# Kernel optimization log

Measured on AMD Instinct MI355X. Metric: run time of the kernel, lower is better.

The kernel has to match this reference:

```python
import jax, jax.numpy as jnp
import numpy as np

W_REG = 3.0
N_CAND = 4
IOU_LEN = 15.0
BIG_COST = 1e8


def focal_cost(cls_pred, gt_labels, alpha=0.25, gamma=2.0, eps=1e-12):
    # cls_pred: [B,P,C] logits, gt_labels: [B,T] int -> [B,P,T]
    p = jax.nn.sigmoid(cls_pred)
    neg = -jnp.log(1.0 - p + eps) * (1.0 - alpha) * p ** gamma
    pos = -jnp.log(p + eps) * alpha * (1.0 - p) ** gamma
    B, P, _ = cls_pred.shape
    T = gt_labels.shape[1]
    idx = jnp.broadcast_to(gt_labels[:, None, :], (B, P, T))
    return jnp.take_along_axis(pos, idx, axis=2) - jnp.take_along_axis(neg, idx, axis=2)


def line_iou(pred, target, img_w, length=IOU_LEN):
    # pred: [B,P,O], target: [B,T,O] -> [B,P,T] (unaligned)
    px1, px2 = pred - length, pred + length
    tx1, tx2 = target - length, target + length
    ovr = jnp.minimum(px2[:, :, None, :], tx2[:, None, :, :]) - jnp.maximum(px1[:, :, None, :], tx1[:, None, :, :])
    union = jnp.maximum(px2[:, :, None, :], tx2[:, None, :, :]) - jnp.minimum(px1[:, :, None, :], tx1[:, None, :, :])
    invalid = ((target < 0) | (target >= img_w))[:, None, :, :]
    ovr = jnp.where(invalid, 0.0, ovr)
    union = jnp.where(invalid, 0.0, union)
    return ovr.sum(-1) / (union.sum(-1) + 1e-9)


def clrnet_assign(preds, targets, masks, img_w, img_h):
    B, P, _ = preds.shape
    T = targets.shape[1]
    w = float(img_w - 1)
    h = float(img_h - 1)
    pa = preds.at[..., 3].multiply(w).at[..., 6:].multiply(w)
    ta = targets.at[..., 3].multiply(w).at[..., 6:].multiply(w)
    p_off, t_off = pa[..., 6:], ta[..., 6:]

    # --- distance score (masked mean L1 over valid target x-offsets) ---
    tvalid = (t_off >= 0) & (t_off < img_w)                      # [B,T,O]
    cmask = tvalid[:, None, :, :]                                 # [B,1,T,O]
    clen = jnp.maximum(cmask.sum(-1).astype(pa.dtype), 1.0)      # [B,1,T]
    diff = jnp.abs(p_off[:, :, None, :] - t_off[:, None, :, :]) * cmask  # [B,P,T,O]
    distances = diff.sum(-1) / clen                               # [B,P,T]
    dist_max = jnp.maximum(distances.max(axis=(1, 2), keepdims=True), 1e-8)
    dist_score = 1.0 - distances / dist_max + 0.01

    # --- start-point score (euclidean on (y*(h), x)) ---
    ps = pa[..., 2:4].at[..., 0].multiply(h)
    ts = ta[..., 2:4].at[..., 0].multiply(h)
    start_d = jnp.sqrt(((ps[:, :, None, :] - ts[:, None, :, :]) ** 2).sum(-1))
    start_max = jnp.maximum(start_d.max(axis=(1, 2), keepdims=True), 1e-8)
    start_score = 1.0 - start_d / start_max + 0.01

    # --- theta score ---
    th_d = jnp.abs(pa[..., 4][:, :, None] - ta[..., 4][:, None, :]) * 180.0
    th_max = jnp.maximum(th_d.max(axis=(1, 2), keepdims=True), 1e-8)
    th_score = 1.0 - th_d / th_max + 0.01

    # --- total cost ---
    gt_labels = ta[..., 1].astype(jnp.int32)
    cls_cost = focal_cost(pa[..., :2], gt_labels)
    reg = (jnp.maximum(dist_score, 1e-3) * jnp.maximum(start_score, 1e-3)
           * jnp.maximum(th_score, 1e-3))
    total_cost = -(reg ** 2) * W_REG + cls_cost                   # [B,P,T]
    valid_t = (masks > 0)[:, None, :]                             # [B,1,T]
    total_cost = jnp.where(valid_t, total_cost, BIG_COST)

    # --- dynamic-k from line IoU ---
    liou = jnp.nan_to_num(line_iou(p_off, t_off, img_w), nan=0.0)
    liou = jnp.where(valid_t, liou, 0.0)
    k = min(N_CAND, P)
    topk_ious, _ = jax.lax.top_k(jnp.swapaxes(liou, 1, 2), k)     # [B,T,k]
    dynamic_ks = jnp.maximum(topk_ious.sum(-1).astype(jnp.int32), 1)
    dynamic_ks = jnp.where(masks > 0, dynamic_ks, 0)              # [B,T]

    # --- top-k lowest-cost priors per target, scatter into matching matrix ---
    _, topk_idx = jax.lax.top_k(-jnp.swapaxes(total_cost, 1, 2), k)  # [B,T,k]
    sel = (jnp.arange(k)[None, None, :] < dynamic_ks[:, :, None]).astype(total_cost.dtype)  # [B,T,k]
    one_hot_p = jax.nn.one_hot(topk_idx, P, dtype=total_cost.dtype)  # [B,T,k,P]
    matching = jnp.swapaxes((one_hot_p * sel[..., None]).sum(2), 1, 2)  # [B,P,T]

    # --- conflict resolution: a prior matched to >1 targets keeps argmin-cost one ---
    conflict = matching.sum(-1) > 1                               # [B,P]
    masked_cost = jnp.where(matching == 0, jnp.inf, total_cost)
    best_t = jnp.argmin(masked_cost, axis=2)                      # [B,P]
    new_m = jax.nn.one_hot(best_t, T, dtype=matching.dtype)
    matching = jnp.where(conflict[..., None], new_m, matching)

    has_match = matching.sum(-1) > 0.5
    t_idx = jnp.argmax(matching, axis=2)
    matched = jnp.where(has_match, t_idx, -1).astype(jnp.int32)
    return matched >= 0, matched


def setup_inputs() -> dict:
    key = jax.random.key(0)
    k1, k2, k3 = jax.random.split(key, 3)
    B, P, T, O = 32, 1000, 16, 72
    D = 6 + O
    preds = jax.random.uniform(k1, (B, P, D), dtype=jnp.float32)
    # slightly outside [0,1] so the invalid-offset masking path is exercised
    targets = jax.random.uniform(k2, (B, T, D), dtype=jnp.float32, minval=-0.05, maxval=1.05)
    masks = jax.random.randint(k3, (B, T), 0, 2).astype(jnp.int32)
    return {"preds": preds, "targets": targets, "masks": masks, "img_w": 800, "img_h": 320}


def reference(preds, targets, masks, img_w, img_h):
    return clrnet_assign(preds, targets, masks, img_w, img_h)
```

## Files before the change

kernel.cpp:

```cpp
#include <hip/hip_runtime.h>
#include <math.h>

#define B_ 32
#define P_ 1000
#define T_ 16
#define D_ 78
#define O_ 72
#define NXB 16
#define BIGC 100000000.0f

__global__ __launch_bounds__(256) void k1(
        const float* __restrict__ preds, const float* __restrict__ targets,
        const int* __restrict__ imgw_p, const int* __restrict__ imgh_p,
        float* __restrict__ Sarr, float4* __restrict__ scal4, float* __restrict__ pths,
        float* __restrict__ pmax, float* __restrict__ cntg) {
    __shared__ float pred_s[64 * 81];
    __shared__ float2 tomg[T_ * O_];
    __shared__ float wmax[4][3];
    __shared__ float cnt_s[T_], clen_s[T_], ts0_s[T_], ts1_s[T_], tth_s[T_];

    const int b = blockIdx.y, bx = blockIdx.x;
    const int p0 = bx * 64;
    const int rows = min(64, P_ - p0);
    const int tid = threadIdx.x;
    const float w = (float)(imgw_p[0] - 1);
    const float h = (float)(imgh_p[0] - 1);
    const float imgwf = (float)imgw_p[0];

    {
        const float4* gbase = (const float4*)(preds + ((size_t)b * P_ + p0) * D_);
        const int n4 = rows * D_ / 4;
        for (int i = tid; i < n4; i += 256) {
            float4 v = gbase[i];
            int base = i * 4;
            int r = base / D_, c = base - r * D_;
#pragma unroll
            for (int k = 0; k < 4; ++k) {
                int cc = c + k, rr = r;
                if (cc >= D_) { cc -= D_; ++rr; }
                float x = (&v.x)[k];
                if (cc >= 6 || cc == 3) x *= w;
                pred_s[rr * 81 + cc] = x;
            }
        }
    }
    for (int i = tid; i < T_ * O_; i += 256) {
        int t = i / O_, o = i - t * O_;
        float to = targets[((size_t)b * T_ + t) * D_ + 6 + o] * w;
        float m = (to >= 0.f && to < imgwf) ? 1.f : 0.f;
        tomg[((t >> 2) * O_ + o) * 4 + (t & 3)] = make_float2(to, m);
    }
    __syncthreads();
    if (tid < T_) {
        int t = tid;
        float c = 0.f;
        for (int o = 0; o < O_; ++o) c += tomg[((t >> 2) * O_ + o) * 4 + (t & 3)].y;
        cnt_s[t] = c;
        clen_s[t] = fmaxf(c, 1.f);
        const float* tr = targets + ((size_t)b * T_ + t) * D_;
        ts0_s[t] = tr[2] * h;
        ts1_s[t] = tr[3] * w;
        tth_s[t] = tr[4];
    }
    __syncthreads();

    if (bx == 0 && tid < T_) cntg[b * T_ + tid] = cnt_s[tid];

    const int lane = tid & 63;
    const int tg = tid >> 6;
    const int p = p0 + lane;

    float ldm = 0.f, lsm = 0.f, ltm = 0.f;
    if (p < P_) {
        const float* lrow = pred_s + lane * 81;
        const float4* tg4 = (const float4*)(tomg + (size_t)tg * O_ * 4);
        float S0 = 0.f, S1 = 0.f, S2 = 0.f, S3 = 0.f;
#pragma unroll 4
        for (int o = 0; o < O_; ++o) {
            float po = lrow[6 + o];
            float4 r0 = tg4[2 * o];
            float4 r1 = tg4[2 * o + 1];
            S0 += r0.y * fabsf(po - r0.x);
            S1 += r0.w * fabsf(po - r0.z);
            S2 += r1.y * fabsf(po - r1.x);
            S3 += r1.w * fabsf(po - r1.z);
        }
        float Sv[4] = {S0, S1, S2, S3};
        float ps0 = lrow[2] * h, ps1 = lrow[3], pth = lrow[4];
#pragma unroll
        for (int j = 0; j < 4; ++j) {
            int t = 4 * tg + j;
            float S = Sv[j];
            Sarr[(size_t)(b * T_ + t) * P_ + p] = S;
            float dv = S / clen_s[t];
            ldm = fmaxf(ldm, dv);
            float d0 = ps0 - ts0_s[t], d1 = ps1 - ts1_s[t];
            lsm = fmaxf(lsm, sqrtf(d0 * d0 + d1 * d1));
            ltm = fmaxf(ltm, fabsf(pth - tth_s[t]) * 180.f);
        }
        if (tg == 0) {
            float fc[2];
#pragma unroll
            for (int c = 0; c < 2; ++c) {
                float x = lrow[c];
                float pc = 1.f / (1.f + expf(-x));
                float neg = -logf(1.f - pc + 1e-12f) * 0.75f * pc * pc;
                float pos = -logf(pc + 1e-12f) * 0.25f * (1.f - pc) * (1.f - pc);
                fc[c] = pos - neg;
            }
            scal4[(size_t)b * P_ + p] = make_float4(fc[0], fc[1], ps0, ps1);
            pths[(size_t)b * P_ + p] = pth;
        }
    }

    for (int off = 32; off; off >>= 1) {
        ldm = fmaxf(ldm, __shfl_xor(ldm, off, 64));
        lsm = fmaxf(lsm, __shfl_xor(lsm, off, 64));
        ltm = fmaxf(ltm, __shfl_xor(ltm, off, 64));
    }
    if (lane == 0) { wmax[tg][0] = ldm; wmax[tg][1] = lsm; wmax[tg][2] = ltm; }
    __syncthreads();
    if (tid == 0) {
        float m0 = 0.f, m1 = 0.f, m2 = 0.f;
#pragma unroll
        for (int i = 0; i < 4; ++i) {
            m0 = fmaxf(m0, wmax[i][0]);
            m1 = fmaxf(m1, wmax[i][1]);
            m2 = fmaxf(m2, wmax[i][2]);
        }
        float* q = pmax + (size_t)(b * NXB + bx) * 3;
        q[0] = m0; q[1] = m1; q[2] = m2;
    }
}

__global__ __launch_bounds__(256) void k2(
        const float* __restrict__ targets, const int* __restrict__ masks,
        const int* __restrict__ imgw_p, const int* __restrict__ imgh_p,
        const float* __restrict__ Sarr,
        const float4* __restrict__ scal4, const float* __restrict__ pths,
        const float* __restrict__ pmax, const float* __restrict__ cntg,
        int4* __restrict__ sel, float4* __restrict__ selc) {
    __shared__ float costL[1024];
    __shared__ float SL[1024];

    const int wid = blockIdx.x;
    const int b = wid >> 4, t = wid & 15;
    const int tid = threadIdx.x;

    float dm = 0.f, sm = 0.f, tm = 0.f;
    for (int i = 0; i < NXB; ++i) {
        const float* q = pmax + (size_t)(b * NXB + i) * 3;
        dm = fmaxf(dm, q[0]); sm = fmaxf(sm, q[1]); tm = fmaxf(tm, q[2]);
    }
    dm = fmaxf(dm, 1e-8f); sm = fmaxf(sm, 1e-8f); tm = fmaxf(tm, 1e-8f);

    const float w = (float)(imgw_p[0] - 1);
    const float h = (float)(imgh_p[0] - 1);
    const float* tr = targets + (size_t)(b * T_ + t) * D_;
    const float ts0 = tr[2] * h, ts1 = tr[3] * w, tth = tr[4];
    int lab = (int)tr[1]; lab = lab < 0 ? 0 : (lab > 1 ? 1 : lab);
    const int mk = masks[b * T_ + t];
    const float cntv = cntg[b * T_ + t];
    const float clen = fmaxf(cntv, 1.f);
    const float c30 = 30.f * cntv;

    const float* Srow = Sarr + (size_t)(b * T_ + t) * P_;
    const float4* s4b = scal4 + (size_t)b * P_;
    const float* ptb = pths + (size_t)b * P_;

#pragma unroll
    for (int i = 0; i < 4; ++i) {
        int p = tid + 256 * i;
        if (p < P_) {
            float S = Srow[p];
            float4 s4 = s4b[p];
            float pth = ptb[p];
            float dv = S / clen;
            float dsc = 1.f - dv / dm + 0.01f;
            float d0 = s4.z - ts0, d1 = s4.w - ts1;
            float ssc = 1.f - sqrtf(d0 * d0 + d1 * d1) / sm + 0.01f;
            float tsc = 1.f - fabsf(pth - tth) * 180.f / tm + 0.01f;
            float reg = fmaxf(dsc, 1e-3f) * fmaxf(ssc, 1e-3f) * fmaxf(tsc, 1e-3f);
            float c = -(reg * reg) * 3.f + (lab ? s4.y : s4.x);
            if (mk <= 0) c = BIGC;
            costL[p] = c;
            SL[p] = S;
        } else {
            costL[p] = INFINITY;
            SL[p] = INFINITY;
        }
    }
    __syncthreads();
    if (tid >= 64) return;

    const int lane = tid;

    float v0, v1, v2, v3;
#define SROUND(vr) { float bv = INFINITY; int bi = 0x7fffffff;            \
        _Pragma("unroll")                                                 \
        for (int i = 0; i < 16; ++i) { int ix = lane + 64 * i;            \
            float v = SL[ix];                                             \
            if (v < bv || (v == bv && ix < bi)) { bv = v; bi = ix; } }    \
        for (int off = 32; off; off >>= 1) {                              \
            float ov = __shfl_xor(bv, off, 64);                           \
            int oi = __shfl_xor(bi, off, 64);                             \
            if (ov < bv || (ov == bv && oi < bi)) { bv = ov; bi = oi; }   \
        }                                                                 \
        vr = bv; if ((bi & 63) == lane) SL[bi] = INFINITY; }
    SROUND(v0) SROUND(v1) SROUND(v2) SROUND(v3)
#undef SROUND
    float l0 = (c30 - v0) / (c30 + v0 + 1e-9f);
    float l1 = (c30 - v1) / (c30 + v1 + 1e-9f);
    float l2 = (c30 - v2) / (c30 + v2 + 1e-9f);
    float l3 = (c30 - v3) / (c30 + v3 + 1e-9f);
    float sum = ((l0 + l1) + l2) + l3;
    int dk = 0;
    if (mk > 0) {
        dk = (int)sum;
        if (dk < 1) dk = 1;
        if (dk > 4) dk = 4;
    }

    int s0, s1, s2, s3;
    float c0, c1, c2, c3;
#define CROUND(sr, cr) { float bv = INFINITY; int bi = 0x7fffffff;        \
        _Pragma("unroll")                                                 \
        for (int i = 0; i < 16; ++i) { int ix = lane + 64 * i;            \
            float v = costL[ix];                                          \
            if (v < bv || (v == bv && ix < bi)) { bv = v; bi = ix; } }    \
        for (int off = 32; off; off >>= 1) {                              \
            float ov = __shfl_xor(bv, off, 64);                           \
            int oi = __shfl_xor(bi, off, 64);                             \
            if (ov < bv || (ov == bv && oi < bi)) { bv = ov; bi = oi; }   \
        }                                                                 \
        sr = bi; cr = bv; if ((bi & 63) == lane) costL[bi] = INFINITY; }
    CROUND(s0, c0) CROUND(s1, c1) CROUND(s2, c2) CROUND(s3, c3)
#undef CROUND

    if (lane == 0) {
        sel[wid]  = make_int4(dk > 0 ? s0 : -1, dk > 1 ? s1 : -1,
                              dk > 2 ? s2 : -1, dk > 3 ? s3 : -1);
        selc[wid] = make_float4(c0, c1, c2, c3);
    }
}

__global__ __launch_bounds__(256) void k3(const int* __restrict__ sel,
                                          const float* __restrict__ selc,
                                          int* __restrict__ out) {
    __shared__ int selE[64];
    __shared__ float selC[64];
    const int b = blockIdx.y, cx = blockIdx.x;
    if (threadIdx.x < 64) {
        selE[threadIdx.x] = sel[b * 64 + threadIdx.x];
        selC[threadIdx.x] = selc[b * 64 + threadIdx.x];
    }
    __syncthreads();

    const int p = cx * 250 + threadIdx.x;
    if (threadIdx.x < 250) {
        int matched = -1;
        float best = INFINITY;
#pragma unroll
        for (int t = 0; t < T_; ++t) {
#pragma unroll
            for (int j = 0; j < 4; ++j) {
                if (selE[4 * t + j] == p) {
                    float c = selC[4 * t + j];
                    if (c < best) { best = c; matched = t; }
                }
            }
        }
        out[b * P_ + p] = (matched >= 0) ? 1 : 0;
        out[B_ * P_ + b * P_ + p] = matched;
    }
}

extern "C" void kernel_launch(void* const* d_in, const int* in_sizes, int n_in,
                              void* d_out, int out_size, void* d_ws, size_t ws_size,
                              hipStream_t stream) {
    const float* preds   = (const float*)d_in[0];
    const float* targets = (const float*)d_in[1];
    const int*   masks   = (const int*)d_in[2];
    const int*   imgw    = (const int*)d_in[3];
    const int*   imgh    = (const int*)d_in[4];
    int* out = (int*)d_out;

    char* ws = (char*)d_ws;
    float*  Sarr  = (float*)ws;
    float4* scal4 = (float4*)(ws + 2048000);
    float*  pths  = (float*)(ws + 2560000);
    float*  pmax  = (float*)(ws + 2688000);
    float*  cntg  = (float*)(ws + 2694144);
    int4*   sel   = (int4*)(ws + 2696192);
    float4* selc  = (float4*)(ws + 2704384);

    k1<<<dim3(NXB, B_), 256, 0, stream>>>(preds, targets, imgw, imgh,
                                          Sarr, scal4, pths, pmax, cntg);
    k2<<<B_ * T_, 256, 0, stream>>>(targets, masks, imgw, imgh, Sarr, scal4, pths,
                                    pmax, cntg, sel, selc);
    k3<<<dim3(4, B_), 256, 0, stream>>>((const int*)sel, (const float*)selc, out);
}
```

Measured before the change: 35.38 us.

## Fuse three kernels into one cooperative kernel with grid-wide syncs

```diff
diff --git a/kernel.cpp b/kernel.cpp
--- a/kernel.cpp
+++ b/kernel.cpp
@@ -1,5 +1,8 @@
 #include <hip/hip_runtime.h>
+#include <hip/hip_cooperative_groups.h>
 #include <math.h>
+
+namespace cg = cooperative_groups;
 
 #define B_ 32
 #define P_ 1000
@@ -9,269 +12,275 @@
 #define NXB 16
 #define BIGC 100000000.0f
 
-__global__ __launch_bounds__(256) void k1(
+__global__ __launch_bounds__(256, 2) void kfused(
         const float* __restrict__ preds, const float* __restrict__ targets,
+        const int* __restrict__ masks,
         const int* __restrict__ imgw_p, const int* __restrict__ imgh_p,
         float* __restrict__ Sarr, float4* __restrict__ scal4, float* __restrict__ pths,
-        float* __restrict__ pmax, float* __restrict__ cntg) {
-    __shared__ float pred_s[64 * 81];
-    __shared__ float2 tomg[T_ * O_];
-    __shared__ float wmax[4][3];
-    __shared__ float cnt_s[T_], clen_s[T_], ts0_s[T_], ts1_s[T_], tth_s[T_];
-
-    const int b = blockIdx.y, bx = blockIdx.x;
-    const int p0 = bx * 64;
-    const int rows = min(64, P_ - p0);
+        float* __restrict__ pmax, float* __restrict__ cntg,
+        int4* __restrict__ sel, float4* __restrict__ selc,
+        int* __restrict__ out) {
+    cg::grid_group grid = cg::this_grid();
+    __shared__ __align__(16) float smem[8192];
+
+    const int g = blockIdx.x;
     const int tid = threadIdx.x;
     const float w = (float)(imgw_p[0] - 1);
     const float h = (float)(imgh_p[0] - 1);
-    const float imgwf = (float)imgw_p[0];
 
     {
-        const float4* gbase = (const float4*)(preds + ((size_t)b * P_ + p0) * D_);
-        const int n4 = rows * D_ / 4;
-        for (int i = tid; i < n4; i += 256) {
-            float4 v = gbase[i];
-            int base = i * 4;
-            int r = base / D_, c = base - r * D_;
-#pragma unroll
-            for (int k = 0; k < 4; ++k) {
-                int cc = c + k, rr = r;
-                if (cc >= D_) { cc -= D_; ++rr; }
-                float x = (&v.x)[k];
-                if (cc >= 6 || cc == 3) x *= w;
-                pred_s[rr * 81 + cc] = x;
-            }
+        float*  pred_s = smem;
+        float2* tomg   = (float2*)(smem + 5184);
+        float*  cnt_s  = smem + 5184 + 2304;
+        float*  clen_s = cnt_s + 16;
+        float*  ts0_s  = clen_s + 16;
+        float*  ts1_s  = ts0_s + 16;
+        float*  tth_s  = ts1_s + 16;
+        float*  wmaxf  = tth_s + 16;
+
+        const int b = g >> 4, bx = g & 15;
+        const int p0 = bx * 64;
+        const int rows = min(64, P_ - p0);
+        const float imgwf = (float)imgw_p[0];
+
+        {
+            const float4* gbase = (const float4*)(preds + ((size_t)b * P_ + p0) * D_);
+            const int n4 = rows * D_ / 4;
+            for (int i = tid; i < n4; i += 256) {
+                float4 v = gbase[i];
+                int base = i * 4;
+                int r = base / D_, c = base - r * D_;
+#pragma unroll
+                for (int k = 0; k < 4; ++k) {
+                    int cc = c + k, rr = r;
+                    if (cc >= D_) { cc -= D_; ++rr; }
+                    float x = (&v.x)[k];
+                    if (cc >= 6 || cc == 3) x *= w;
+                    pred_s[rr * 81 + cc] = x;
+                }
+            }
+        }
+        for (int i = tid; i < T_ * O_; i += 256) {
+            int t = i / O_, o = i - t * O_;
+            float to = targets[((size_t)b * T_ + t) * D_ + 6 + o] * w;
+            float m = (to >= 0.f && to < imgwf) ? 1.f : 0.f;
+            tomg[((t >> 2) * O_ + o) * 4 + (t & 3)] = make_float2(to, m);
+        }
+        __syncthreads();
+        if (tid < T_) {
+            int t = tid;
+            float c = 0.f;
+            for (int o = 0; o < O_; ++o) c += tomg[((t >> 2) * O_ + o) * 4 + (t & 3)].y;
+            cnt_s[t] = c;
+            clen_s[t] = fmaxf(c, 1.f);
+            const float* tr = targets + ((size_t)b * T_ + t) * D_;
+            ts0_s[t] = tr[2] * h;
+            ts1_s[t] = tr[3] * w;
+            tth_s[t] = tr[4];
+        }
+        __syncthreads();
+
+        if (bx == 0 && tid < T_) cntg[b * T_ + tid] = cnt_s[tid];
+
+        const int lane = tid & 63;
+        const int tg = tid >> 6;
+        const int p = p0 + lane;
+
+        float ldm = 0.f, lsm = 0.f, ltm = 0.f;
+        if (p < P_) {
+            const float* lrow = pred_s + lane * 81;
+            const float4* tg4 = (const float4*)(tomg + (size_t)tg * O_ * 4);
+            float S0 = 0.f, S1 = 0.f, S2 = 0.f, S3 = 0.f;
+#pragma unroll 4
+            for (int o = 0; o < O_; ++o) {
+                float po = lrow[6 + o];
+                float4 r0 = tg4[2 * o];
+                float4 r1 = tg4[2 * o + 1];
+                S0 += r0.y * fabsf(po - r0.x);
+                S1 += r0.w * fabsf(po - r0.z);
+                S2 += r1.y * fabsf(po - r1.x);
+                S3 += r1.w * fabsf(po - r1.z);
+            }
+            float Sv[4] = {S0, S1, S2, S3};
+            float ps0 = lrow[2] * h, ps1 = lrow[3], pth = lrow[4];
+#pragma unroll
+            for (int j = 0; j < 4; ++j) {
+                int t = 4 * tg + j;
+                float S = Sv[j];
+                Sarr[(size_t)(b * T_ + t) * P_ + p] = S;
+                float dv = S / clen_s[t];
+                ldm = fmaxf(ldm, dv);
+                float d0 = ps0 - ts0_s[t], d1 = ps1 - ts1_s[t];
+                lsm = fmaxf(lsm, sqrtf(d0 * d0 + d1 * d1));
+                ltm = fmaxf(ltm, fabsf(pth - tth_s[t]) * 180.f);
+            }
+            if (tg == 0) {
+                float fc[2];
+#pragma unroll
+                for (int c = 0; c < 2; ++c) {
+                    float x = lrow[c];
+                    float pc = 1.f / (1.f + expf(-x));
+                    float neg = -logf(1.f - pc + 1e-12f) * 0.75f * pc * pc;
+                    float pos = -logf(pc + 1e-12f) * 0.25f * (1.f - pc) * (1.f - pc);
+                    fc[c] = pos - neg;
+                }
+                scal4[(size_t)b * P_ + p] = make_float4(fc[0], fc[1], ps0, ps1);
+                pths[(size_t)b * P_ + p] = pth;
+            }
+        }
+
+        for (int off = 32; off; off >>= 1) {
+            ldm = fmaxf(ldm, __shfl_xor(ldm, off, 64));
+            lsm = fmaxf(lsm, __shfl_xor(lsm, off, 64));
+            ltm = fmaxf(ltm, __shfl_xor(ltm, off, 64));
+        }
+        if (lane == 0) { wmaxf[tg * 3 + 0] = ldm; wmaxf[tg * 3 + 1] = lsm; wmaxf[tg * 3 + 2] = ltm; }
+        __syncthreads();
+        if (tid == 0) {
+            float m0 = 0.f, m1 = 0.f, m2 = 0.f;
+#pragma unroll
+            for (int i = 0; i < 4; ++i) {
+                m0 = fmaxf(m0, wmaxf[i * 3 + 0]);
+                m1 = fmaxf(m1, wmaxf[i * 3 + 1]);
+                m2 = fmaxf(m2, wmaxf[i * 3 + 2]);
+            }
+            float* q = pmax + (size_t)(b * NXB + bx) * 3;
+            q[0] = m0; q[1] = m1; q[2] = m2;
         }
     }
-    for (int i = tid; i < T_ * O_; i += 256) {
-        int t = i / O_, o = i - t * O_;
-        float to = targets[((size_t)b * T_ + t) * D_ + 6 + o] * w;
-        float m = (to >= 0.f && to < imgwf) ? 1.f : 0.f;
-        tomg[((t >> 2) * O_ + o) * 4 + (t & 3)] = make_float2(to, m);
+
+    grid.sync();
+
+    {
+        float* costL = smem;
+        float* SL    = smem + 1024;
+
+        const int b = g >> 4, t = g & 15;
+
+        float dm = 0.f, sm = 0.f, tm = 0.f;
+        for (int i = 0; i < NXB; ++i) {
+            const float* q = pmax + (size_t)(b * NXB + i) * 3;
+            dm = fmaxf(dm, q[0]); sm = fmaxf(sm, q[1]); tm = fmaxf(tm, q[2]);
+        }
+        dm = fmaxf(dm, 1e-8f); sm = fmaxf(sm, 1e-8f); tm = fmaxf(tm, 1e-8f);
+
+        const float* tr = targets + (size_t)(b * T_ + t) * D_;
+        const float ts0 = tr[2] * h, ts1 = tr[3] * w, tth = tr[4];
+        int lab = (int)tr[1]; lab = lab < 0 ? 0 : (lab > 1 ? 1 : lab);
+        const int mk = masks[b * T_ + t];
+        const float cntv = cntg[b * T_ + t];
+        const float clen = fmaxf(cntv, 1.f);
+        const float c30 = 30.f * cntv;
+
+        const float* Srow = Sarr + (size_t)(b * T_ + t) * P_;
+        const float4* s4b = scal4 + (size_t)b * P_;
+        const float* ptb = pths + (size_t)b * P_;
+
+#pragma unroll
+        for (int i = 0; i < 4; ++i) {
+            int p = tid + 256 * i;
+            if (p < P_) {
+                float S = Srow[p];
+                float4 s4 = s4b[p];
+                float pth = ptb[p];
+                float dv = S / clen;
+                float dsc = 1.f - dv / dm + 0.01f;
+                float d0 = s4.z - ts0, d1 = s4.w - ts1;
+                float ssc = 1.f - sqrtf(d0 * d0 + d1 * d1) / sm + 0.01f;
+                float tsc = 1.f - fabsf(pth - tth) * 180.f / tm + 0.01f;
+                float reg = fmaxf(dsc, 1e-3f) * fmaxf(ssc, 1e-3f) * fmaxf(tsc, 1e-3f);
+                float c = -(reg * reg) * 3.f + (lab ? s4.y : s4.x);
+                if (mk <= 0) c = BIGC;
+                costL[p] = c;
+                SL[p] = S;
+            } else {
+                costL[p] = INFINITY;
+                SL[p] = INFINITY;
+            }
+        }
+        __syncthreads();
+
+        if (tid < 64) {
+            const int lane = tid;
+
+            float v0, v1, v2, v3;
+#define SROUND(vr) { float bv = INFINITY; int bi = 0x7fffffff;            \
+            _Pragma("unroll")                                             \
+            for (int i = 0; i < 16; ++i) { int ix = lane + 64 * i;        \
+                float v = SL[ix];                                         \
+                if (v < bv || (v == bv && ix < bi)) { bv = v; bi = ix; } }\
+            for (int off = 32; off; off >>= 1) {                          \
+                float ov = __shfl_xor(bv, off, 64);                       \
+                int oi = __shfl_xor(bi, off, 64);                         \
+                if (ov < bv || (ov == bv && oi < bi)) { bv = ov; bi = oi; } } \
+            vr = bv; if ((bi & 63) == lane) SL[bi] = INFINITY; }
+            SROUND(v0) SROUND(v1) SROUND(v2) SROUND(v3)
+#undef SROUND
+            float l0 = (c30 - v0) / (c30 + v0 + 1e-9f);
+            float l1 = (c30 - v1) / (c30 + v1 + 1e-9f);
+            float l2 = (c30 - v2) / (c30 + v2 + 1e-9f);
+            float l3 = (c30 - v3) / (c30 + v3 + 1e-9f);
+            float sum = ((l0 + l1) + l2) + l3;
+            int dk = 0;
+            if (mk > 0) {
+                dk = (int)sum;
+                if (dk < 1) dk = 1;
+                if (dk > 4) dk = 4;
+            }
+
+            int s0, s1, s2, s3;
+            float c0, c1, c2, c3;
+#define CROUND(sr, cr) { float bv = INFINITY; int bi = 0x7fffffff;        \
+            _Pragma("unroll")                                             \
+            for (int i = 0; i < 16; ++i) { int ix = lane + 64 * i;        \
+                float v = costL[ix];                                      \
+                if (v < bv || (v == bv && ix < bi)) { bv = v; bi = ix; } }\
+            for (int off = 32; off; off >>= 1) {                          \
+                float ov = __shfl_xor(bv, off, 64);                       \
+                int oi = __shfl_xor(bi, off, 64);                         \
+                if (ov < bv || (ov == bv && oi < bi)) { bv = ov; bi = oi; } } \
+            sr = bi; cr = bv; if ((bi & 63) == lane) costL[bi] = INFINITY; }
+            CROUND(s0, c0) CROUND(s1, c1) CROUND(s2, c2) CROUND(s3, c3)
+#undef CROUND
+
+            if (lane == 0) {
+                sel[g]  = make_int4(dk > 0 ? s0 : -1, dk > 1 ? s1 : -1,
+                                    dk > 2 ? s2 : -1, dk > 3 ? s3 : -1);
+                selc[g] = make_float4(c0, c1, c2, c3);
+            }
+        }
     }
-    __syncthreads();
-    if (tid < T_) {
-        int t = tid;
-        float c = 0.f;
-        for (int o = 0; o < O_; ++o) c += tomg[((t >> 2) * O_ + o) * 4 + (t & 3)].y;
-        cnt_s[t] = c;
-        clen_s[t] = fmaxf(c, 1.f);
-        const float* tr = targets + ((size_t)b * T_ + t) * D_;
-        ts0_s[t] = tr[2] * h;
-        ts1_s[t] = tr[3] * w;
-        tth_s[t] = tr[4];
-    }
-    __syncthreads();
-
-    if (bx == 0 && tid < T_) cntg[b * T_ + tid] = cnt_s[tid];
-
-    const int lane = tid & 63;
-    const int tg = tid >> 6;
-    const int p = p0 + lane;
-
-    float ldm = 0.f, lsm = 0.f, ltm = 0.f;
-    if (p < P_) {
-        const float* lrow = pred_s + lane * 81;
-        const float4* tg4 = (const float4*)(tomg + (size_t)tg * O_ * 4);
-        float S0 = 0.f, S1 = 0.f, S2 = 0.f, S3 = 0.f;
-#pragma unroll 4
-        for (int o = 0; o < O_; ++o) {
-            float po = lrow[6 + o];
-            float4 r0 = tg4[2 * o];
-            float4 r1 = tg4[2 * o + 1];
-            S0 += r0.y * fabsf(po - r0.x);
-            S1 += r0.w * fabsf(po - r0.z);
-            S2 += r1.y * fabsf(po - r1.x);
-            S3 += r1.w * fabsf(po - r1.z);
-        }
-        float Sv[4] = {S0, S1, S2, S3};
-        float ps0 = lrow[2] * h, ps1 = lrow[3], pth = lrow[4];
-#pragma unroll
-        for (int j = 0; j < 4; ++j) {
-            int t = 4 * tg + j;
-            float S = Sv[j];
-            Sarr[(size_t)(b * T_ + t) * P_ + p] = S;
-            float dv = S / clen_s[t];
-            ldm = fmaxf(ldm, dv);
-            float d0 = ps0 - ts0_s[t], d1 = ps1 - ts1_s[t];
-            lsm = fmaxf(lsm, sqrtf(d0 * d0 + d1 * d1));
-            ltm = fmaxf(ltm, fabsf(pth - tth_s[t]) * 180.f);
-        }
-        if (tg == 0) {
-            float fc[2];
-#pragma unroll
-            for (int c = 0; c < 2; ++c) {
-                float x = lrow[c];
-                float pc = 1.f / (1.f + expf(-x));
-                float neg = -logf(1.f - pc + 1e-12f) * 0.75f * pc * pc;
-                float pos = -logf(pc + 1e-12f) * 0.25f * (1.f - pc) * (1.f - pc);
-                fc[c] = pos - neg;
-            }
-            scal4[(size_t)b * P_ + p] = make_float4(fc[0], fc[1], ps0, ps1);
-            pths[(size_t)b * P_ + p] = pth;
-        }
-    }
-
-    for (int off = 32; off; off >>= 1) {
-        ldm = fmaxf(ldm, __shfl_xor(ldm, off, 64));
-        lsm = fmaxf(lsm, __shfl_xor(lsm, off, 64));
-        ltm = fmaxf(ltm, __shfl_xor(ltm, off, 64));
-    }
-    if (lane == 0) { wmax[tg][0] = ldm; wmax[tg][1] = lsm; wmax[tg][2] = ltm; }
-    __syncthreads();
-    if (tid == 0) {
-        float m0 = 0.f, m1 = 0.f, m2 = 0.f;
-#pragma unroll
-        for (int i = 0; i < 4; ++i) {
-            m0 = fmaxf(m0, wmax[i][0]);
-            m1 = fmaxf(m1, wmax[i][1]);
-            m2 = fmaxf(m2, wmax[i][2]);
-        }
-        float* q = pmax + (size_t)(b * NXB + bx) * 3;
-        q[0] = m0; q[1] = m1; q[2] = m2;
-    }
-}
-
-__global__ __launch_bounds__(256) void k2(
-        const float* __restrict__ targets, const int* __restrict__ masks,
-        const int* __restrict__ imgw_p, const int* __restrict__ imgh_p,
-        const float* __restrict__ Sarr,
-        const float4* __restrict__ scal4, const float* __restrict__ pths,
-        const float* __restrict__ pmax, const float* __restrict__ cntg,
-        int4* __restrict__ sel, float4* __restrict__ selc) {
-    __shared__ float costL[1024];
-    __shared__ float SL[1024];
-
-    const int wid = blockIdx.x;
-    const int b = wid >> 4, t = wid & 15;
-    const int tid = threadIdx.x;
-
-    float dm = 0.f, sm = 0.f, tm = 0.f;
-    for (int i = 0; i < NXB; ++i) {
-        const float* q = pmax + (size_t)(b * NXB + i) * 3;
-        dm = fmaxf(dm, q[0]); sm = fmaxf(sm, q[1]); tm = fmaxf(tm, q[2]);
-    }
-    dm = fmaxf(dm, 1e-8f); sm = fmaxf(sm, 1e-8f); tm = fmaxf(tm, 1e-8f);
-
-    const float w = (float)(imgw_p[0] - 1);
-    const float h = (float)(imgh_p[0] - 1);
-    const float* tr = targets + (size_t)(b * T_ + t) * D_;
-    const float ts0 = tr[2] * h, ts1 = tr[3] * w, tth = tr[4];
-    int lab = (int)tr[1]; lab = lab < 0 ? 0 : (lab > 1 ? 1 : lab);
-    const int mk = masks[b * T_ + t];
-    const float cntv = cntg[b * T_ + t];
-    const float clen = fmaxf(cntv, 1.f);
-    const float c30 = 30.f * cntv;
-
-    const float* Srow = Sarr + (size_t)(b * T_ + t) * P_;
-    const float4* s4b = scal4 + (size_t)b * P_;
-    const float* ptb = pths + (size_t)b * P_;
-
-#pragma unroll
-    for (int i = 0; i < 4; ++i) {
-        int p = tid + 256 * i;
-        if (p < P_) {
-            float S = Srow[p];
-            float4 s4 = s4b[p];
-            float pth = ptb[p];
-            float dv = S / clen;
-            float dsc = 1.f - dv / dm + 0.01f;
-            float d0 = s4.z - ts0, d1 = s4.w - ts1;
-            float ssc = 1.f - sqrtf(d0 * d0 + d1 * d1) / sm + 0.01f;
-            float tsc = 1.f - fabsf(pth - tth) * 180.f / tm + 0.01f;
-            float reg = fmaxf(dsc, 1e-3f) * fmaxf(ssc, 1e-3f) * fmaxf(tsc, 1e-3f);
-            float c = -(reg * reg) * 3.f + (lab ? s4.y : s4.x);
-            if (mk <= 0) c = BIGC;
-            costL[p] = c;
-            SL[p] = S;
-        } else {
-            costL[p] = INFINITY;
-            SL[p] = INFINITY;
-        }
-    }
-    __syncthreads();
-    if (tid >= 64) return;
-
-    const int lane = tid;
-
-    float v0, v1, v2, v3;
-#define SROUND(vr) { float bv = INFINITY; int bi = 0x7fffffff;            \
-        _Pragma("unroll")                                                 \
-        for (int i = 0; i < 16; ++i) { int ix = lane + 64 * i;            \
-            float v = SL[ix];                                             \
-            if (v < bv || (v == bv && ix < bi)) { bv = v; bi = ix; } }    \
-        for (int off = 32; off; off >>= 1) {                              \
-            float ov = __shfl_xor(bv, off, 64);                           \
-            int oi = __shfl_xor(bi, off, 64);                             \
-            if (ov < bv || (ov == bv && oi < bi)) { bv = ov; bi = oi; }   \
-        }                                                                 \
-        vr = bv; if ((bi & 63) == lane) SL[bi] = INFINITY; }
-    SROUND(v0) SROUND(v1) SROUND(v2) SROUND(v3)
-#undef SROUND
-    float l0 = (c30 - v0) / (c30 + v0 + 1e-9f);
-    float l1 = (c30 - v1) / (c30 + v1 + 1e-9f);
-    float l2 = (c30 - v2) / (c30 + v2 + 1e-9f);
-    float l3 = (c30 - v3) / (c30 + v3 + 1e-9f);
-    float sum = ((l0 + l1) + l2) + l3;
-    int dk = 0;
-    if (mk > 0) {
-        dk = (int)sum;
-        if (dk < 1) dk = 1;
-        if (dk > 4) dk = 4;
-    }
-
-    int s0, s1, s2, s3;
-    float c0, c1, c2, c3;
-#define CROUND(sr, cr) { float bv = INFINITY; int bi = 0x7fffffff;        \
-        _Pragma("unroll")                                                 \
-        for (int i = 0; i < 16; ++i) { int ix = lane + 64 * i;            \
-            float v = costL[ix];                                          \
-            if (v < bv || (v == bv && ix < bi)) { bv = v; bi = ix; } }    \
-        for (int off = 32; off; off >>= 1) {                              \
-            float ov = __shfl_xor(bv, off, 64);                           \
-            int oi = __shfl_xor(bi, off, 64);                             \
-            if (ov < bv || (ov == bv && oi < bi)) { bv = ov; bi = oi; }   \
-        }                                                                 \
-        sr = bi; cr = bv; if ((bi & 63) == lane) costL[bi] = INFINITY; }
-    CROUND(s0, c0) CROUND(s1, c1) CROUND(s2, c2) CROUND(s3, c3)
-#undef CROUND
-
-    if (lane == 0) {
-        sel[wid]  = make_int4(dk > 0 ? s0 : -1, dk > 1 ? s1 : -1,
-                              dk > 2 ? s2 : -1, dk > 3 ? s3 : -1);
-        selc[wid] = make_float4(c0, c1, c2, c3);
-    }
-}
-
-__global__ __launch_bounds__(256) void k3(const int* __restrict__ sel,
-                                          const float* __restrict__ selc,
-                                          int* __restrict__ out) {
-    __shared__ int selE[64];
-    __shared__ float selC[64];
-    const int b = blockIdx.y, cx = blockIdx.x;
-    if (threadIdx.x < 64) {
-        selE[threadIdx.x] = sel[b * 64 + threadIdx.x];
-        selC[threadIdx.x] = selc[b * 64 + threadIdx.x];
-    }
-    __syncthreads();
-
-    const int p = cx * 250 + threadIdx.x;
-    if (threadIdx.x < 250) {
-        int matched = -1;
-        float best = INFINITY;
-#pragma unroll
-        for (int t = 0; t < T_; ++t) {
-#pragma unroll
-            for (int j = 0; j < 4; ++j) {
-                if (selE[4 * t + j] == p) {
-                    float c = selC[4 * t + j];
-                    if (c < best) { best = c; matched = t; }
+
+    grid.sync();
+
+    if (g < 128) {
+        int*   selE = (int*)smem;
+        float* selC = smem + 64;
+
+        const int b = g >> 2, cx = g & 3;
+        if (tid < 64) {
+            selE[tid] = ((const int*)sel)[b * 64 + tid];
+            selC[tid] = ((const float*)selc)[b * 64 + tid];
+        }
+        __syncthreads();
+
+        const int p = cx * 250 + tid;
+        if (tid < 250) {
+            int matched = -1;
+            float best = INFINITY;
+#pragma unroll
+            for (int t = 0; t < T_; ++t) {
+#pragma unroll
+                for (int j = 0; j < 4; ++j) {
+                    if (selE[4 * t + j] == p) {
+                        float c = selC[4 * t + j];
+                        if (c < best) { best = c; matched = t; }
+                    }
                 }
             }
-        }
-        out[b * P_ + p] = (matched >= 0) ? 1 : 0;
-        out[B_ * P_ + b * P_ + p] = matched;
+            out[b * P_ + p] = (matched >= 0) ? 1 : 0;
+            out[B_ * P_ + b * P_ + p] = matched;
+        }
     }
 }
 
@@ -294,9 +303,10 @@
     int4*   sel   = (int4*)(ws + 2696192);
     float4* selc  = (float4*)(ws + 2704384);
 
-    k1<<<dim3(NXB, B_), 256, 0, stream>>>(preds, targets, imgw, imgh,
-                                          Sarr, scal4, pths, pmax, cntg);
-    k2<<<B_ * T_, 256, 0, stream>>>(targets, masks, imgw, imgh, Sarr, scal4, pths,
-                                    pmax, cntg, sel, selc);
-    k3<<<dim3(4, B_), 256, 0, stream>>>((const int*)sel, (const float*)selc, out);
+    void* args[] = {
+        (void*)&preds, (void*)&targets, (void*)&masks, (void*)&imgw, (void*)&imgh,
+        (void*)&Sarr, (void*)&scal4, (void*)&pths, (void*)&pmax, (void*)&cntg,
+        (void*)&sel, (void*)&selc, (void*)&out
+    };
+    hipLaunchCooperativeKernel((void*)kfused, dim3(512), dim3(256), args, 0, stream);
 }
```

After: 128.6 us. +263.4%, slower.
